# Kernel tuning notes

Hardware: AMD Instinct MI355X
Metric: run time of the kernel (lower is better)

## Reference

```python
import jax, jax.numpy as jnp
import numpy as np

NUM_HEADS = 16
VALUE_SIZE = 64
MODEL_SIZE = 1024
BATCH = 4
SEQ = 1024


def setup_inputs() -> dict:
    key = jax.random.key(0)
    ks = jax.random.split(key, 5)
    scale = 1.0 / np.sqrt(MODEL_SIZE)
    x = jax.random.normal(ks[0], (BATCH, SEQ, MODEL_SIZE), dtype=jnp.float32)
    w_q = jax.random.normal(ks[1], (MODEL_SIZE, NUM_HEADS * VALUE_SIZE), dtype=jnp.float32) * scale
    w_kv = jax.random.normal(ks[2], (MODEL_SIZE, NUM_HEADS * VALUE_SIZE), dtype=jnp.float32) * scale
    w_o = jax.random.normal(ks[3], (NUM_HEADS * VALUE_SIZE, MODEL_SIZE), dtype=jnp.float32) * scale
    # original init is Constant(0.0); use small random values for a non-trivial test
    k_weights = jax.random.normal(ks[4], (1, NUM_HEADS, 1, VALUE_SIZE), dtype=jnp.float32) * 0.02
    return {"x": x, "w_q": w_q, "w_kv": w_kv, "w_o": w_o, "k_weights": k_weights}


def reference(x, w_q, w_kv, w_o, k_weights):
    b, L, d = x.shape
    h, v = NUM_HEADS, VALUE_SIZE
    # projections (no bias); q scaled by 1/sqrt(model_size)
    q = (x @ w_q) * (1.0 / jnp.sqrt(jnp.asarray(d, x.dtype)))
    q = q.reshape(b, L, h, v).transpose(0, 2, 1, 3)    # b h l v
    kv = (x @ w_kv).reshape(b, L, h, v).transpose(0, 2, 1, 3)  # b h l v
    # learned per-head key scaling on the shared k=v tensor
    k = kv * (1.0 + k_weights)
    logits = jnp.einsum('bhik,bhjk->bhij', q, k)       # b h L L
    mask = jnp.tril(jnp.ones((L, L), dtype=bool))
    logits = jnp.where(mask, logits, jnp.asarray(-1e6, logits.dtype))
    a = jax.nn.softmax(logits, axis=-1)
    y = jnp.einsum('bhij,bhjv->bhiv', a, kv)           # attend over shared kv
    y = y.transpose(0, 2, 1, 3).reshape(b, L, h * v)
    return y @ w_o
```

## Files before the change

### kernel.cpp

```cpp
#include <hip/hip_runtime.h>
#include <hip/hip_bf16.h>
#include <stdint.h>

#define BATCH 4
#define SEQ   1024
#define DMODEL 1024
#define NH    16
#define DV    64

typedef short bf8 __attribute__((ext_vector_type(8)));
typedef float f4  __attribute__((ext_vector_type(4)));

static __device__ __forceinline__ short f2bf(float f) {
    union { float f; uint32_t u; } a; a.f = f;
    uint32_t r = a.u + 0x7FFF + ((a.u >> 16) & 1);
    return (short)(r >> 16);
}

static __device__ __forceinline__ f4 mfma16(bf8 a, bf8 b, f4 c) {
    return __builtin_amdgcn_mfma_f32_16x16x32_bf16(a, b, c, 0, 0, 0);
}

static __device__ __forceinline__ void gload16(const short* g, short* l) {
    __builtin_amdgcn_global_load_lds((const __attribute__((address_space(1))) void*)g,
                                     (__attribute__((address_space(3))) void*)l,
                                     16, 0, 0);
}


__global__ void prep_kernel(const float* __restrict__ x,
                            const float* __restrict__ wq, const float* __restrict__ wkv,
                            const float* __restrict__ wo,
                            short* __restrict__ xb,
                            short* __restrict__ wqkvt, short* __restrict__ wot) {
    int z = blockIdx.z;
    int tx = threadIdx.x, ty = threadIdx.y;
    if (z >= 3) {
        int i = (((z - 3) * 1024 + blockIdx.y * 32 + blockIdx.x) << 8) + ty * 32 + tx;
        float4 v = ((const float4*)x)[i];
        short4 o;
        o.x = f2bf(v.x); o.y = f2bf(v.y); o.z = f2bf(v.z); o.w = f2bf(v.w);
        ((short4*)xb)[i] = o;
        return;
    }
    __shared__ float tile[32][33];
    const float* w = (z == 0) ? wq : (z == 1) ? wkv : wo;
    short* wt = (z == 0) ? wqkvt : (z == 1) ? (wqkvt + (1u << 20)) : wot;
    int bx = blockIdx.x, by = blockIdx.y;
    #pragma unroll
    for (int i = 0; i < 4; i++)
        tile[ty + i * 8][tx] = w[(size_t)(by * 32 + ty + i * 8) * 1024 + bx * 32 + tx];
    __syncthreads();
    #pragma unroll
    for (int i = 0; i < 4; i++)
        wt[(size_t)(bx * 32 + ty + i * 8) * 1024 + by * 32 + tx] = f2bf(tile[tx][ty + i * 8]);
}


__global__ __launch_bounds__(256) void gemm_proj_kernel(
    const short* __restrict__ A, const short* __restrict__ Bt,
    const float* __restrict__ kw,
    short* __restrict__ q_out, short* __restrict__ kv_out, short* __restrict__ kvT_out)
{
    __shared__ short SM[32768];
    const int K = DMODEL;

    int tid = threadIdx.x;
    int wave = tid >> 6, lane = tid & 63;
    int quad = lane >> 4, l16 = lane & 15;
    int m0 = blockIdx.y * 128;
    int n0 = blockIdx.x * 128;
    int wm = (wave >> 1) * 64;
    int wn = (wave & 1) * 64;
    int sw = l16 & 7;

    f4 acc[4][4] = {};

    auto stage = [&](int buf, int k0) {
        short* As = SM + buf * 16384;
        short* Bs = As + 8192;
        #pragma unroll
        for (int c = 0; c < 4; c++) {
            int flat = c * 256 + tid;
            int row = flat >> 3;
            int seg = (flat & 7) ^ (row & 7);
            gload16(A + (size_t)(m0 + row) * K + k0 + seg * 8, As + flat * 8);
        }
        #pragma unroll
        for (int c = 0; c < 4; c++) {
            int flat = c * 256 + tid;
            int row = flat >> 3;
            int seg = (flat & 7) ^ (row & 7);
            gload16(Bt + (size_t)(n0 + row) * K + k0 + seg * 8, Bs + flat * 8);
        }
    };

    stage(0, 0);
    for (int k0 = 0; k0 < K; k0 += 64) {
        int buf = (k0 >> 6) & 1;
        __syncthreads();
        if (k0 + 64 < K) stage(buf ^ 1, k0 + 64);
        const short* As = SM + buf * 16384;
        const short* Bs = As + 8192;
        #pragma unroll
        for (int kk = 0; kk < 2; kk++) {
            bf8 ar[4], br[4];
            #pragma unroll
            for (int i = 0; i < 4; i++)
                ar[i] = *(const bf8*)(As + (wm + i * 16 + l16) * 64 + ((kk * 4 + quad) ^ sw) * 8);
            #pragma unroll
            for (int j = 0; j < 4; j++)
                br[j] = *(const bf8*)(Bs + (wn + j * 16 + l16) * 64 + ((kk * 4 + quad) ^ sw) * 8);
            #pragma unroll
            for (int i = 0; i < 4; i++) {
                #pragma unroll
                for (int j = 0; j < 4; j++)
                    acc[i][j] = mfma16(ar[i], br[j], acc[i][j]);
            }
        }
    }

    if (n0 < 1024) {
        #pragma unroll
        for (int j = 0; j < 4; j++) {
            int n = n0 + wn + j * 16 + l16;
            float kws = 0.03125f * (1.0f + kw[n]);
            #pragma unroll
            for (int i = 0; i < 4; i++) {
                int mb = m0 + wm + i * 16 + quad * 4;
                q_out[(size_t)(mb + 0) * 1024 + n] = f2bf(acc[i][j][0] * kws);
                q_out[(size_t)(mb + 1) * 1024 + n] = f2bf(acc[i][j][1] * kws);
                q_out[(size_t)(mb + 2) * 1024 + n] = f2bf(acc[i][j][2] * kws);
                q_out[(size_t)(mb + 3) * 1024 + n] = f2bf(acc[i][j][3] * kws);
            }
        }
        return;
    }

    #pragma unroll
    for (int j = 0; j < 4; j++) {
        int n2 = n0 - 1024 + wn + j * 16 + l16;
        #pragma unroll
        for (int i = 0; i < 4; i++) {
            int mb = m0 + wm + i * 16 + quad * 4;
            kv_out[(size_t)(mb + 0) * 1024 + n2] = f2bf(acc[i][j][0]);
            kv_out[(size_t)(mb + 1) * 1024 + n2] = f2bf(acc[i][j][1]);
            kv_out[(size_t)(mb + 2) * 1024 + n2] = f2bf(acc[i][j][2]);
            kv_out[(size_t)(mb + 3) * 1024 + n2] = f2bf(acc[i][j][3]);
        }
    }

    {
        const int TST = 136;
        short* T = SM;
        __syncthreads();
        short* Tw = T + (wave & 1) * (64 * TST);
        #pragma unroll
        for (int j = 0; j < 4; j++) {
            int nl = j * 16 + l16;
            #pragma unroll
            for (int i = 0; i < 4; i++) {
                short4 tv;
                tv.x = f2bf(acc[i][j][0]); tv.y = f2bf(acc[i][j][1]);
                tv.z = f2bf(acc[i][j][2]); tv.w = f2bf(acc[i][j][3]);
                *(short4*)(Tw + nl * TST + wm + i * 16 + quad * 4) = tv;
            }
        }
        __syncthreads();
        int n2base = n0 - 1024;
        int mloc = m0 & 1023;
        int bq = m0 >> 10;
        #pragma unroll
        for (int c = 0; c < 8; c++) {
            int flat = c * 256 + tid;
            int row = flat >> 4;
            int seg = flat & 15;
            bf8 vseg = *(const bf8*)(T + (row >> 6) * (64 * TST) + (row & 63) * TST + seg * 8);
            int n2 = n2base + row;
            int bh = (bq << 4) + (n2 >> 6);
            *(bf8*)(kvT_out + (size_t)(bh * 64 + (n2 & 63)) * 1024 + mloc + seg * 8) = vseg;
        }
    }
}


__global__ __launch_bounds__(256) void gemm_out_kernel(
    const short* __restrict__ A, const short* __restrict__ Bt,
    float* __restrict__ c_out)
{
    __shared__ short SM[32768];
    const int K = DMODEL;

    int tid = threadIdx.x;
    int wave = tid >> 6, lane = tid & 63;
    int quad = lane >> 4, l16 = lane & 15;
    int m0 = blockIdx.y * 128;
    int n0 = blockIdx.x * 128;
    int wm = (wave >> 1) * 64;
    int wn = (wave & 1) * 64;
    int sw = l16 & 7;

    f4 acc[4][4] = {};

    auto stage = [&](int buf, int k0) {
        short* As = SM + buf * 16384;
        short* Bs = As + 8192;
        #pragma unroll
        for (int c = 0; c < 4; c++) {
            int flat = c * 256 + tid;
            int row = flat >> 3;
            int seg = (flat & 7) ^ (row & 7);
            gload16(A + (size_t)(m0 + row) * K + k0 + seg * 8, As + flat * 8);
        }
        #pragma unroll
        for (int c = 0; c < 4; c++) {
            int flat = c * 256 + tid;
            int row = flat >> 3;
            int seg = (flat & 7) ^ (row & 7);
            gload16(Bt + (size_t)(n0 + row) * K + k0 + seg * 8, Bs + flat * 8);
        }
    };

    stage(0, 0);
    for (int k0 = 0; k0 < K; k0 += 64) {
        int buf = (k0 >> 6) & 1;
        __syncthreads();
        if (k0 + 64 < K) stage(buf ^ 1, k0 + 64);
        const short* As = SM + buf * 16384;
        const short* Bs = As + 8192;
        #pragma unroll
        for (int kk = 0; kk < 2; kk++) {
            bf8 ar[4], br[4];
            #pragma unroll
            for (int i = 0; i < 4; i++)
                ar[i] = *(const bf8*)(As + (wm + i * 16 + l16) * 64 + ((kk * 4 + quad) ^ sw) * 8);
            #pragma unroll
            for (int j = 0; j < 4; j++)
                br[j] = *(const bf8*)(Bs + (wn + j * 16 + l16) * 64 + ((kk * 4 + quad) ^ sw) * 8);
            #pragma unroll
            for (int i = 0; i < 4; i++) {
                #pragma unroll
                for (int j = 0; j < 4; j++)
                    acc[i][j] = mfma16(ar[i], br[j], acc[i][j]);
            }
        }
    }

    #pragma unroll
    for (int j = 0; j < 4; j++) {
        int n = n0 + wn + j * 16 + l16;
        #pragma unroll
        for (int i = 0; i < 4; i++) {
            int mb = m0 + wm + i * 16 + quad * 4;
            c_out[(size_t)(mb + 0) * 1024 + n] = acc[i][j][0];
            c_out[(size_t)(mb + 1) * 1024 + n] = acc[i][j][1];
            c_out[(size_t)(mb + 2) * 1024 + n] = acc[i][j][2];
            c_out[(size_t)(mb + 3) * 1024 + n] = acc[i][j][3];
        }
    }
}


#define PLD 72

__global__ __launch_bounds__(256) void attn_kernel(
    const short* __restrict__ qg, const short* __restrict__ kvg,
    const short* __restrict__ kvTg, short* __restrict__ yg)
{
    int bh = blockIdx.y;
    int b = bh >> 4, h = bh & 15;
    int x = blockIdx.x;
    int tid = threadIdx.x;
    int wave = tid >> 6, lane = tid & 63;
    int quad = lane >> 4, l16 = lane & 15;
    int qa0 = x * 64;
    int qb0 = (15 - x) * 64;
    int ntiles = 16 - x;

    __shared__ short Ks[2][64 * 64];
    __shared__ short Vs[2][64 * 64];
    __shared__ short Ps[4][2 * 16 * PLD];
    short* myPB = &Ps[wave][0];
    short* myPA = &Ps[wave][16 * PLD];

    const short* qpa = qg + (size_t)(b * 1024 + qa0 + wave * 16 + l16) * 1024 + h * 64;
    const short* qpb = qg + (size_t)(b * 1024 + qb0 + wave * 16 + l16) * 1024 + h * 64;
    bf8 qa_0 = *(const bf8*)(qpa + quad * 8);
    bf8 qa_1 = *(const bf8*)(qpa + 32 + quad * 8);
    bf8 qb_0 = *(const bf8*)(qpb + quad * 8);
    bf8 qb_1 = *(const bf8*)(qpb + 32 + quad * 8);

    bf8 ones;
    #pragma unroll
    for (int j = 0; j < 8; j++) ones[j] = (short)0x3F80;

    f4 oa[4] = {}, ob[4] = {};
    f4 lsa = {}, lsb = {};
    int rowbaseA = qa0 + wave * 16 + quad * 4;
    int rowbaseB = qb0 + wave * 16 + quad * 4;

    auto stage = [&](int jt) {
        short* dstK = &Ks[jt & 1][0];
        short* dstV = &Vs[jt & 1][0];
        int j0 = jt * 64;
        #pragma unroll
        for (int k = 0; k < 2; k++) {
            int flat = k * 256 + tid;
            int row = flat >> 3;
            int lseg = (flat & 7) ^ (row & 7);
            gload16(kvg + (size_t)(b * 1024 + j0 + row) * 1024 + h * 64 + lseg * 8,
                    dstK + flat * 8);
            gload16(kvTg + (size_t)(bh * 64 + row) * 1024 + j0 + lseg * 8,
                    dstV + flat * 8);
        }
    };

    auto qk = [&](bf8 qf0, bf8 qf1, const short* K, f4 (&s)[4]) {
        #pragma unroll
        for (int c = 0; c < 4; c++) {
            int row = c * 16 + l16;
            int swz = row & 7;
            bf8 kb0 = *(const bf8*)(K + row * 64 + (quad ^ swz) * 8);
            bf8 kb1 = *(const bf8*)(K + row * 64 + (((quad + 4) ^ swz)) * 8);
            f4 t = {};
            t = mfma16(qf0, kb0, t);
            t = mfma16(qf1, kb1, t);
            s[c] = t;
        }
    };

    auto expstore = [&](f4 (&s)[4], int rowbase, int j0, short* P) {
        #pragma unroll
        for (int r = 0; r < 4; r++) {
            int qi = rowbase + r;
            float p0 = (j0 + l16      <= qi) ? __expf(s[0][r]) : 0.0f;
            float p1 = (j0 + 16 + l16 <= qi) ? __expf(s[1][r]) : 0.0f;
            float p2 = (j0 + 32 + l16 <= qi) ? __expf(s[2][r]) : 0.0f;
            float p3 = (j0 + 48 + l16 <= qi) ? __expf(s[3][r]) : 0.0f;
            int prow = quad * 4 + r;
            P[prow * PLD + l16]      = f2bf(p0);
            P[prow * PLD + 16 + l16] = f2bf(p1);
            P[prow * PLD + 32 + l16] = f2bf(p2);
            P[prow * PLD + 48 + l16] = f2bf(p3);
        }
    };

    auto pv = [&](const short* P, const short* V, f4 (&o)[4], f4& lsum) {
        bf8 pf0 = *(const bf8*)(P + l16 * PLD + quad * 8);
        bf8 pf1 = *(const bf8*)(P + l16 * PLD + 32 + quad * 8);
        lsum = mfma16(pf0, ones, lsum);
        lsum = mfma16(pf1, ones, lsum);
        #pragma unroll
        for (int t = 0; t < 4; t++) {
            int vrow = t * 16 + l16;
            int swz = vrow & 7;
            bf8 vb0 = *(const bf8*)(V + vrow * 64 + (quad ^ swz) * 8);
            bf8 vb1 = *(const bf8*)(V + vrow * 64 + (((quad + 4) ^ swz)) * 8);
            o[t] = mfma16(pf0, vb0, o[t]);
            o[t] = mfma16(pf1, vb1, o[t]);
        }
    };

    stage(0);

    for (int jt = 0; jt < ntiles; jt++) {
        __syncthreads();
        if (jt + 1 < ntiles) stage(jt + 1);
        const short* K = &Ks[jt & 1][0];
        const short* V = &Vs[jt & 1][0];
        int j0 = jt * 64;
        bool doA = (jt <= x);

        if (doA) {
            f4 sb[4], sa[4];
            #pragma unroll
            for (int c = 0; c < 4; c++) {
                int row = c * 16 + l16;
                int swz = row & 7;
                bf8 kb0 = *(const bf8*)(K + row * 64 + (quad ^ swz) * 8);
                bf8 kb1 = *(const bf8*)(K + row * 64 + (((quad + 4) ^ swz)) * 8);
                f4 tb = {};
                tb = mfma16(qb_0, kb0, tb);
                tb = mfma16(qb_1, kb1, tb);
                sb[c] = tb;
                f4 ta = {};
                ta = mfma16(qa_0, kb0, ta);
                ta = mfma16(qa_1, kb1, ta);
                sa[c] = ta;
            }
            expstore(sb, rowbaseB, j0, myPB);
            expstore(sa, rowbaseA, j0, myPA);
            bf8 pb0 = *(const bf8*)(myPB + l16 * PLD + quad * 8);
            bf8 pb1 = *(const bf8*)(myPB + l16 * PLD + 32 + quad * 8);
            bf8 pa0 = *(const bf8*)(myPA + l16 * PLD + quad * 8);
            bf8 pa1 = *(const bf8*)(myPA + l16 * PLD + 32 + quad * 8);
            lsb = mfma16(pb0, ones, lsb);
            lsb = mfma16(pb1, ones, lsb);
            lsa = mfma16(pa0, ones, lsa);
            lsa = mfma16(pa1, ones, lsa);
            #pragma unroll
            for (int t = 0; t < 4; t++) {
                int vrow = t * 16 + l16;
                int swz = vrow & 7;
                bf8 vb0 = *(const bf8*)(V + vrow * 64 + (quad ^ swz) * 8);
                bf8 vb1 = *(const bf8*)(V + vrow * 64 + (((quad + 4) ^ swz)) * 8);
                ob[t] = mfma16(pb0, vb0, ob[t]);
                ob[t] = mfma16(pb1, vb1, ob[t]);
                oa[t] = mfma16(pa0, vb0, oa[t]);
                oa[t] = mfma16(pa1, vb1, oa[t]);
            }
        } else {
            f4 sb[4];
            qk(qb_0, qb_1, K, sb);
            expstore(sb, rowbaseB, j0, myPB);
            pv(myPB, V, ob, lsb);
        }
    }

    {
        float r0 = 1.0f / lsa[0], r1 = 1.0f / lsa[1], r2 = 1.0f / lsa[2], r3 = 1.0f / lsa[3];
        #pragma unroll
        for (int t = 0; t < 4; t++) {
            size_t base = (size_t)(b * SEQ + rowbaseA) * (NH * DV) + h * DV + t * 16 + l16;
            yg[base]                 = f2bf(oa[t][0] * r0);
            yg[base + 1 * (NH * DV)] = f2bf(oa[t][1] * r1);
            yg[base + 2 * (NH * DV)] = f2bf(oa[t][2] * r2);
            yg[base + 3 * (NH * DV)] = f2bf(oa[t][3] * r3);
        }
    }
    {
        float r0 = 1.0f / lsb[0], r1 = 1.0f / lsb[1], r2 = 1.0f / lsb[2], r3 = 1.0f / lsb[3];
        #pragma unroll
        for (int t = 0; t < 4; t++) {
            size_t base = (size_t)(b * SEQ + rowbaseB) * (NH * DV) + h * DV + t * 16 + l16;
            yg[base]                 = f2bf(ob[t][0] * r0);
            yg[base + 1 * (NH * DV)] = f2bf(ob[t][1] * r1);
            yg[base + 2 * (NH * DV)] = f2bf(ob[t][2] * r2);
            yg[base + 3 * (NH * DV)] = f2bf(ob[t][3] * r3);
        }
    }
}


extern "C" void kernel_launch(void* const* d_in, const int* in_sizes, int n_in,
                              void* d_out, int out_size, void* d_ws, size_t ws_size,
                              hipStream_t stream) {
    const float* x    = (const float*)d_in[0];
    const float* w_q  = (const float*)d_in[1];
    const float* w_kv = (const float*)d_in[2];
    const float* w_o  = (const float*)d_in[3];
    const float* kw   = (const float*)d_in[4];
    float* out = (float*)d_out;

    char* ws = (char*)d_ws;
    short* xb    = (short*)(ws);
    short* wqkvt = (short*)(ws + ( 8u << 20));
    short* wot   = (short*)(ws + (12u << 20));
    short* qp    = (short*)(ws + (14u << 20));
    short* kvb   = (short*)(ws + (22u << 20));
    short* kvT   = (short*)(ws + (30u << 20));
    short* yb    = (short*)(ws + (38u << 20));

    prep_kernel<<<dim3(32, 32, 7), dim3(32, 8), 0, stream>>>(
        x, w_q, w_kv, w_o, xb, wqkvt, wot);

    gemm_proj_kernel<<<dim3(16, 32), 256, 0, stream>>>(
        xb, wqkvt, kw, qp, kvb, kvT);

    attn_kernel<<<dim3(8, BATCH * NH), 256, 0, stream>>>(qp, kvb, kvT, yb);

    gemm_out_kernel<<<dim3(8, 32), 256, 0, stream>>>(yb, wot, out);
}
```

Before: 145.8 us.

## Switch projection GEMMs to 32x32 MFMA and skip causal mask on interior tiles

Both GEMM kernels now compute each wave's 64x64 tile with four 32x32x16 bf16 MFMAs per k-step instead of sixteen 16x16x32 ones. This reduces LDS fragment loads and instruction count per FLOP, and the epilogue index mapping is rewritten to match the new accumulator layout. The attention kernel applies the causal mask compare only on diagonal tiles and uses an unmasked exp-store path elsewhere. The risks are higher accumulator register pressure and a wrong epilogue mapping if the layout assumptions are off.

```diff
diff --git a/kernel.cpp b/kernel.cpp
--- a/kernel.cpp
+++ b/kernel.cpp
@@ -8,8 +8,9 @@
 #define NH    16
 #define DV    64
 
-typedef short bf8 __attribute__((ext_vector_type(8)));
-typedef float f4  __attribute__((ext_vector_type(4)));
+typedef short bf8  __attribute__((ext_vector_type(8)));
+typedef float f4   __attribute__((ext_vector_type(4)));
+typedef float f16x __attribute__((ext_vector_type(16)));
 
 static __device__ __forceinline__ short f2bf(float f) {
     union { float f; uint32_t u; } a; a.f = f;
@@ -19,6 +20,10 @@
 
 static __device__ __forceinline__ f4 mfma16(bf8 a, bf8 b, f4 c) {
     return __builtin_amdgcn_mfma_f32_16x16x32_bf16(a, b, c, 0, 0, 0);
+}
+
+static __device__ __forceinline__ f16x mfma32(bf8 a, bf8 b, f16x c) {
+    return __builtin_amdgcn_mfma_f32_32x32x16_bf16(a, b, c, 0, 0, 0);
 }
 
 static __device__ __forceinline__ void gload16(const short* g, short* l) {
@@ -67,14 +72,14 @@
 
     int tid = threadIdx.x;
     int wave = tid >> 6, lane = tid & 63;
-    int quad = lane >> 4, l16 = lane & 15;
+    int l32 = lane & 31, half = lane >> 5;
     int m0 = blockIdx.y * 128;
     int n0 = blockIdx.x * 128;
     int wm = (wave >> 1) * 64;
     int wn = (wave & 1) * 64;
-    int sw = l16 & 7;
-
-    f4 acc[4][4] = {};
+    int sw = l32 & 7;
+
+    f16x acc[2][2] = {};
 
     auto stage = [&](int buf, int k0) {
         short* As = SM + buf * 16384;
@@ -103,50 +108,57 @@
         const short* As = SM + buf * 16384;
         const short* Bs = As + 8192;
         #pragma unroll
-        for (int kk = 0; kk < 2; kk++) {
-            bf8 ar[4], br[4];
-            #pragma unroll
-            for (int i = 0; i < 4; i++)
-                ar[i] = *(const bf8*)(As + (wm + i * 16 + l16) * 64 + ((kk * 4 + quad) ^ sw) * 8);
-            #pragma unroll
-            for (int j = 0; j < 4; j++)
-                br[j] = *(const bf8*)(Bs + (wn + j * 16 + l16) * 64 + ((kk * 4 + quad) ^ sw) * 8);
-            #pragma unroll
-            for (int i = 0; i < 4; i++) {
+        for (int ks = 0; ks < 4; ks++) {
+            int seg = (ks * 2 + half) ^ sw;
+            bf8 ar[2], br[2];
+            #pragma unroll
+            for (int i = 0; i < 2; i++)
+                ar[i] = *(const bf8*)(As + (wm + i * 32 + l32) * 64 + seg * 8);
+            #pragma unroll
+            for (int j = 0; j < 2; j++)
+                br[j] = *(const bf8*)(Bs + (wn + j * 32 + l32) * 64 + seg * 8);
+            #pragma unroll
+            for (int i = 0; i < 2; i++) {
                 #pragma unroll
-                for (int j = 0; j < 4; j++)
-                    acc[i][j] = mfma16(ar[i], br[j], acc[i][j]);
+                for (int j = 0; j < 2; j++)
+                    acc[i][j] = mfma32(ar[i], br[j], acc[i][j]);
             }
         }
     }
 
     if (n0 < 1024) {
         #pragma unroll
-        for (int j = 0; j < 4; j++) {
-            int n = n0 + wn + j * 16 + l16;
+        for (int j = 0; j < 2; j++) {
+            int n = n0 + wn + j * 32 + l32;
             float kws = 0.03125f * (1.0f + kw[n]);
             #pragma unroll
-            for (int i = 0; i < 4; i++) {
-                int mb = m0 + wm + i * 16 + quad * 4;
-                q_out[(size_t)(mb + 0) * 1024 + n] = f2bf(acc[i][j][0] * kws);
-                q_out[(size_t)(mb + 1) * 1024 + n] = f2bf(acc[i][j][1] * kws);
-                q_out[(size_t)(mb + 2) * 1024 + n] = f2bf(acc[i][j][2] * kws);
-                q_out[(size_t)(mb + 3) * 1024 + n] = f2bf(acc[i][j][3] * kws);
+            for (int i = 0; i < 2; i++) {
+                int mb = m0 + wm + i * 32 + half * 4;
+                #pragma unroll
+                for (int g = 0; g < 4; g++) {
+                    #pragma unroll
+                    for (int r = 0; r < 4; r++)
+                        q_out[(size_t)(mb + g * 8 + r) * 1024 + n] =
+                            f2bf(acc[i][j][g * 4 + r] * kws);
+                }
             }
         }
         return;
     }
 
     #pragma unroll
-    for (int j = 0; j < 4; j++) {
-        int n2 = n0 - 1024 + wn + j * 16 + l16;
-        #pragma unroll
-        for (int i = 0; i < 4; i++) {
-            int mb = m0 + wm + i * 16 + quad * 4;
-            kv_out[(size_t)(mb + 0) * 1024 + n2] = f2bf(acc[i][j][0]);
-            kv_out[(size_t)(mb + 1) * 1024 + n2] = f2bf(acc[i][j][1]);
-            kv_out[(size_t)(mb + 2) * 1024 + n2] = f2bf(acc[i][j][2]);
-            kv_out[(size_t)(mb + 3) * 1024 + n2] = f2bf(acc[i][j][3]);
+    for (int j = 0; j < 2; j++) {
+        int n2 = n0 - 1024 + wn + j * 32 + l32;
+        #pragma unroll
+        for (int i = 0; i < 2; i++) {
+            int mb = m0 + wm + i * 32 + half * 4;
+            #pragma unroll
+            for (int g = 0; g < 4; g++) {
+                #pragma unroll
+                for (int r = 0; r < 4; r++)
+                    kv_out[(size_t)(mb + g * 8 + r) * 1024 + n2] =
+                        f2bf(acc[i][j][g * 4 + r]);
+            }
         }
     }
 
@@ -156,14 +168,19 @@
         __syncthreads();
         short* Tw = T + (wave & 1) * (64 * TST);
         #pragma unroll
-        for (int j = 0; j < 4; j++) {
-            int nl = j * 16 + l16;
-            #pragma unroll
-            for (int i = 0; i < 4; i++) {
-                short4 tv;
-                tv.x = f2bf(acc[i][j][0]); tv.y = f2bf(acc[i][j][1]);
-                tv.z = f2bf(acc[i][j][2]); tv.w = f2bf(acc[i][j][3]);
-                *(short4*)(Tw + nl * TST + wm + i * 16 + quad * 4) = tv;
+        for (int j = 0; j < 2; j++) {
+            int nl = j * 32 + l32;
+            #pragma unroll
+            for (int i = 0; i < 2; i++) {
+                #pragma unroll
+                for (int g = 0; g < 4; g++) {
+                    short4 tv;
+                    tv.x = f2bf(acc[i][j][g * 4 + 0]);
+                    tv.y = f2bf(acc[i][j][g * 4 + 1]);
+                    tv.z = f2bf(acc[i][j][g * 4 + 2]);
+                    tv.w = f2bf(acc[i][j][g * 4 + 3]);
+                    *(short4*)(Tw + nl * TST + wm + i * 32 + g * 8 + half * 4) = tv;
+                }
             }
         }
         __syncthreads();
@@ -193,14 +210,14 @@
 
     int tid = threadIdx.x;
     int wave = tid >> 6, lane = tid & 63;
-    int quad = lane >> 4, l16 = lane & 15;
+    int l32 = lane & 31, half = lane >> 5;
     int m0 = blockIdx.y * 128;
     int n0 = blockIdx.x * 128;
     int wm = (wave >> 1) * 64;
     int wn = (wave & 1) * 64;
-    int sw = l16 & 7;
-
-    f4 acc[4][4] = {};
+    int sw = l32 & 7;
+
+    f16x acc[2][2] = {};
 
     auto stage = [&](int buf, int k0) {
         short* As = SM + buf * 16384;
@@ -229,33 +246,36 @@
         const short* As = SM + buf * 16384;
         const short* Bs = As + 8192;
         #pragma unroll
-        for (int kk = 0; kk < 2; kk++) {
-            bf8 ar[4], br[4];
-            #pragma unroll
-            for (int i = 0; i < 4; i++)
-                ar[i] = *(const bf8*)(As + (wm + i * 16 + l16) * 64 + ((kk * 4 + quad) ^ sw) * 8);
-            #pragma unroll
-            for (int j = 0; j < 4; j++)
-                br[j] = *(const bf8*)(Bs + (wn + j * 16 + l16) * 64 + ((kk * 4 + quad) ^ sw) * 8);
-            #pragma unroll
-            for (int i = 0; i < 4; i++) {
+        for (int ks = 0; ks < 4; ks++) {
+            int seg = (ks * 2 + half) ^ sw;
+            bf8 ar[2], br[2];
+            #pragma unroll
+            for (int i = 0; i < 2; i++)
+                ar[i] = *(const bf8*)(As + (wm + i * 32 + l32) * 64 + seg * 8);
+            #pragma unroll
+            for (int j = 0; j < 2; j++)
+                br[j] = *(const bf8*)(Bs + (wn + j * 32 + l32) * 64 + seg * 8);
+            #pragma unroll
+            for (int i = 0; i < 2; i++) {
                 #pragma unroll
-                for (int j = 0; j < 4; j++)
-                    acc[i][j] = mfma16(ar[i], br[j], acc[i][j]);
+                for (int j = 0; j < 2; j++)
+                    acc[i][j] = mfma32(ar[i], br[j], acc[i][j]);
             }
         }
     }
 
     #pragma unroll
-    for (int j = 0; j < 4; j++) {
-        int n = n0 + wn + j * 16 + l16;
-        #pragma unroll
-        for (int i = 0; i < 4; i++) {
-            int mb = m0 + wm + i * 16 + quad * 4;
-            c_out[(size_t)(mb + 0) * 1024 + n] = acc[i][j][0];
-            c_out[(size_t)(mb + 1) * 1024 + n] = acc[i][j][1];
-            c_out[(size_t)(mb + 2) * 1024 + n] = acc[i][j][2];
-            c_out[(size_t)(mb + 3) * 1024 + n] = acc[i][j][3];
+    for (int j = 0; j < 2; j++) {
+        int n = n0 + wn + j * 32 + l32;
+        #pragma unroll
+        for (int i = 0; i < 2; i++) {
+            int mb = m0 + wm + i * 32 + half * 4;
+            #pragma unroll
+            for (int g = 0; g < 4; g++) {
+                #pragma unroll
+                for (int r = 0; r < 4; r++)
+                    c_out[(size_t)(mb + g * 8 + r) * 1024 + n] = acc[i][j][g * 4 + r];
+            }
         }
     }
 }
@@ -329,7 +349,18 @@
         }
     };
 
-    auto expstore = [&](f4 (&s)[4], int rowbase, int j0, short* P) {
+    auto expstoreU = [&](f4 (&s)[4], short* P) {
+        #pragma unroll
+        for (int r = 0; r < 4; r++) {
+            int prow = quad * 4 + r;
+            P[prow * PLD + l16]      = f2bf(__expf(s[0][r]));
+            P[prow * PLD + 16 + l16] = f2bf(__expf(s[1][r]));
+            P[prow * PLD + 32 + l16] = f2bf(__expf(s[2][r]));
+            P[prow * PLD + 48 + l16] = f2bf(__expf(s[3][r]));
+        }
+    };
+
+    auto expstoreM = [&](f4 (&s)[4], int rowbase, int j0, short* P) {
         #pragma unroll
         for (int r = 0; r < 4; r++) {
             int qi = rowbase + r;
@@ -388,8 +419,9 @@
                 ta = mfma16(qa_1, kb1, ta);
                 sa[c] = ta;
             }
-            expstore(sb, rowbaseB, j0, myPB);
-            expstore(sa, rowbaseA, j0, myPA);
+            expstoreU(sb, myPB);
+            if (jt == x) expstoreM(sa, rowbaseA, j0, myPA);
+            else         expstoreU(sa, myPA);
             bf8 pb0 = *(const bf8*)(myPB + l16 * PLD + quad * 8);
             bf8 pb1 = *(const bf8*)(myPB + l16 * PLD + 32 + quad * 8);
             bf8 pa0 = *(const bf8*)(myPA + l16 * PLD + quad * 8);
@@ -412,7 +444,8 @@
         } else {
             f4 sb[4];
             qk(qb_0, qb_1, K, sb);
-            expstore(sb, rowbaseB, j0, myPB);
+            if (jt == ntiles - 1) expstoreM(sb, rowbaseB, j0, myPB);
+            else                  expstoreU(sb, myPB);
             pv(myPB, V, ob, lsb);
         }
     }
```

After: 155.4 us. +6.6%, slower.
